# Performance work log

Hardware: AMD Instinct MI355X
Metric: run time of the kernel (lower is better)

## Reference

```python
import jax, jax.numpy as jnp
import numpy as np

D = 1024      # feature_dim / vertice_dim
H = 4         # n_heads
HD = D // H   # head dim 256
DFF = 2 * D   # 2048
DV = 1024     # vertice_dim
T = 64        # frame_num
PERIOD = 30
NEG = -1e9


def setup_inputs() -> dict:
    key = jax.random.key(0)
    ks = iter(jax.random.split(key, 32))
    sc = 0.02
    def w(shape):
        return jax.random.normal(next(ks), shape, dtype=jnp.float32) * sc
    return {
        "hidden_states": jax.random.normal(next(ks), (T, DV), dtype=jnp.float32),
        "hid_w": w((D, DV)), "hid_b": w((D,)),
        "obj_w": w((D, 80)),
        "sa_in_w": w((3 * D, D)), "sa_in_b": w((3 * D,)),
        "sa_out_w": w((D, D)), "sa_out_b": w((D,)),
        "ca_in_w": w((3 * D, D)), "ca_in_b": w((3 * D,)),
        "ca_out_w": w((D, D)), "ca_out_b": w((D,)),
        "ln1_g": jnp.ones((D,), jnp.float32), "ln1_b": jnp.zeros((D,), jnp.float32),
        "ln2_g": jnp.ones((D,), jnp.float32), "ln2_b": jnp.zeros((D,), jnp.float32),
        "ln3_g": jnp.ones((D,), jnp.float32), "ln3_b": jnp.zeros((D,), jnp.float32),
        "ff1_w": w((DFF, D)), "ff1_b": w((DFF,)),
        "ff2_w": w((D, DFF)), "ff2_b": w((D,)),
        "vr_w": w((DV, D)), "vr_b": w((DV,)),
        "vm_w": w((D, DV)), "vm_b": w((D,)),
    }


def _periodic_pe():
    # sin/cos PE over one period, tiled (PeriodicPositionalEncoding)
    pos = jnp.arange(PERIOD, dtype=jnp.float32)[:, None]
    div = jnp.exp(jnp.arange(0, D, 2, dtype=jnp.float32) * (-np.log(10000.0) / D))
    pe = jnp.zeros((PERIOD, D), jnp.float32)
    pe = pe.at[:, 0::2].set(jnp.sin(pos * div)).at[:, 1::2].set(jnp.cos(pos * div))
    reps = T // PERIOD + 1
    return jnp.tile(pe, (reps, 1))[:T]  # (T, D)


def reference(hidden_states, hid_w, hid_b, obj_w,
              sa_in_w, sa_in_b, sa_out_w, sa_out_b,
              ca_in_w, ca_in_b, ca_out_w, ca_out_b,
              ln1_g, ln1_b, ln2_g, ln2_b, ln3_g, ln3_b,
              ff1_w, ff1_b, ff2_w, ff2_b, vr_w, vr_b, vm_w, vm_b):
    mem = hidden_states @ hid_w.T + hid_b          # (S=T, D)
    style = obj_w[:, 0]                             # one-hot(0) @ obj_vector
    pe = _periodic_pe()

    # ALiBi-style biased causal mask (init_biased_mask, n_head=4)
    slopes = 0.25 ** jnp.arange(1, H + 1, dtype=jnp.float32)
    idx = jnp.arange(T)
    i_, j_ = idx[:, None], idx[None, :]
    alibi = -((i_ - j_) // PERIOD).astype(jnp.float32)
    tgt_bias = jnp.where(j_ <= i_, slopes[:, None, None] * alibi[None], NEG)  # (H,T,T)
    # vocaset enc_dec_mask: frame i may only attend memory frame i
    mem_bias = jnp.where(i_ == j_, 0.0, NEG)  # (T,S)

    def mha(q_in, kv_in, in_w, in_b, out_w, out_b, bias):
        wq, wk, wv = jnp.split(in_w, 3, axis=0)
        bq, bk, bv = jnp.split(in_b, 3)
        q = (q_in @ wq.T + bq).reshape(-1, H, HD)
        k = (kv_in @ wk.T + bk).reshape(-1, H, HD)
        v = (kv_in @ wv.T + bv).reshape(-1, H, HD)
        s = jnp.einsum('qhd,khd->hqk', q, k) / np.sqrt(HD) + bias
        a = jax.nn.softmax(s, axis=-1)
        o = jnp.einsum('hqk,khd->qhd', a, v).reshape(-1, D)
        return o @ out_w.T + out_b

    def ln(x, g, b):
        m = x.mean(-1, keepdims=True)
        v = ((x - m) ** 2).mean(-1, keepdims=True)
        return (x - m) / jnp.sqrt(v + 1e-5) * g + b

    def decode(x):  # post-norm TransformerDecoderLayer (eval, dropout off)
        x = ln(x + mha(x, x, sa_in_w, sa_in_b, sa_out_w, sa_out_b, tgt_bias), ln1_g, ln1_b)
        x = ln(x + mha(x, mem, ca_in_w, ca_in_b, ca_out_w, ca_out_b, mem_bias[None]), ln2_g, ln2_b)
        h = jax.nn.relu(x @ ff1_w.T + ff1_b) @ ff2_w.T + ff2_b
        return ln(x + h, ln3_g, ln3_b)

    # independent of the zero-padded future slots, matching the growing-seq loop.
    emb0 = jnp.zeros((T, D), jnp.float32).at[0].set(style)

    def step(emb, i):
        out = decode(emb + pe)
        new_tok = (out[i] @ vr_w.T + vr_b) @ vm_w.T + vm_b + style
        return emb.at[i + 1].set(new_tok), None

    emb, _ = jax.lax.scan(step, emb0, jnp.arange(T - 1))
    # final iteration's vertice_out over the full T-length sequence
    return decode(emb + pe) @ vr_w.T + vr_b  # (T, DV)
```

## Files before the change

### kernel.cpp

```cpp
#include <hip/hip_runtime.h>
#include <math.h>

#define DIM  1024
#define SEQ  64
#define HDIM 256
#define NBLK 256

__device__ __forceinline__ float wsum(float v){
  v += __shfl_xor(v, 32, 64); v += __shfl_xor(v, 16, 64); v += __shfl_xor(v, 8, 64);
  v += __shfl_xor(v, 4, 64);  v += __shfl_xor(v, 2, 64);  v += __shfl_xor(v, 1, 64);
  return v;
}
__device__ __forceinline__ float wmax(float v){
  v = fmaxf(v, __shfl_xor(v, 32, 64)); v = fmaxf(v, __shfl_xor(v, 16, 64));
  v = fmaxf(v, __shfl_xor(v, 8, 64));  v = fmaxf(v, __shfl_xor(v, 4, 64));
  v = fmaxf(v, __shfl_xor(v, 2, 64));  v = fmaxf(v, __shfl_xor(v, 1, 64));
  return v;
}
__device__ __forceinline__ float2 breduce2(float va, float vb, float* red){
  int tid = threadIdx.x;
  va = wsum(va); vb = wsum(vb);
  if ((tid & 63) == 0){ red[(tid >> 6) * 2] = va; red[(tid >> 6) * 2 + 1] = vb; }
  __syncthreads();
  float ra = red[0] + red[2] + red[4] + red[6];
  float rb = red[1] + red[3] + red[5] + red[7];
  __syncthreads();
  return make_float2(ra, rb);
}

__device__ __forceinline__ float ldc(const float* p){
  return __hip_atomic_load(p, __ATOMIC_RELAXED, __HIP_MEMORY_SCOPE_AGENT);
}
__device__ __forceinline__ void stc(float* p, float v){
  __hip_atomic_store(p, v, __ATOMIC_RELAXED, __HIP_MEMORY_SCOPE_AGENT);
}

__device__ __forceinline__ void spin_ge(unsigned* p, unsigned ep){
  unsigned spins = 0;
  while (__hip_atomic_load(p, __ATOMIC_RELAXED, __HIP_MEMORY_SCOPE_AGENT) < ep){
    if (++spins > 4194304u){
      unsigned s2 = 0;
      while (__hip_atomic_load(p, __ATOMIC_ACQUIRE, __HIP_MEMORY_SCOPE_AGENT) < ep){
        __builtin_amdgcn_s_sleep(2);
        if (++s2 > 100000000u) break;
      }
      return;
    }
  }
}

#define SLOT_STRIDE 32
__device__ __forceinline__ void gsync(unsigned* slots, unsigned ep, int bid, int tid){
  asm volatile("s_waitcnt vmcnt(0)" ::: "memory");
  __syncthreads();
  if (tid == 0)
    __hip_atomic_store(&slots[bid * SLOT_STRIDE], ep, __ATOMIC_RELAXED, __HIP_MEMORY_SCOPE_AGENT);
  spin_ge(&slots[tid * SLOT_STRIDE], ep);
  __syncthreads();
  asm volatile("" ::: "memory");
}

__global__ void matmul_nn_1024(const float* __restrict__ A, const float* __restrict__ B,
                               float* __restrict__ Cc){
  __shared__ float As[32][33];
  __shared__ float Bs[32][33];
  int tb = blockIdx.x * 32, ta = blockIdx.y * 32;
  int tx = threadIdx.x & 31, ty = threadIdx.x >> 5;
  float acc[4] = {0.f, 0.f, 0.f, 0.f};
  for (int k0 = 0; k0 < 1024; k0 += 32){
    for (int r = ty; r < 32; r += 8) As[r][tx] = A[(size_t)(ta + r) * 1024 + k0 + tx];
    for (int r = ty; r < 32; r += 8) Bs[r][tx] = B[(size_t)(k0 + r) * 1024 + tb + tx];
    __syncthreads();
    #pragma unroll
    for (int kk = 0; kk < 32; ++kk){
      float bv = Bs[kk][tx];
      #pragma unroll
      for (int m = 0; m < 4; ++m) acc[m] = fmaf(As[ty + 8 * m][kk], bv, acc[m]);
    }
    __syncthreads();
  }
  for (int m = 0; m < 4; ++m) Cc[(size_t)(ta + ty + 8 * m) * 1024 + tb + tx] = acc[m];
}

struct CoopArgs {
  const float *hs, *hid_w, *hid_b;
  const float *sa_in_w, *sa_in_b, *sa_out_w, *sa_out_b;
  const float *ca_in_w, *ca_in_b, *ca_out_w, *ca_out_b;
  const float *ln1_g, *ln1_b, *ln2_g, *ln2_b, *ln3_g, *ln3_b;
  const float *ff1_w, *ff1_b, *ff2_w, *ff2_b;
  const float *vr_w, *vr_b, *vm_w, *vm_b, *obj_w;
  const float *Cm;
  float *pe, *emb, *kc, *vc, *mem, *vtmp, *cac, *q, *u, *hb, *w, *s;
  float *out;
  unsigned *bar;
  unsigned *flags;
};

__global__ void __launch_bounds__(256, 2) decode_loop(CoopArgs a){
  const int tid = threadIdx.x, bid = blockIdx.x;
  const int wave = tid >> 6, lane = tid & 63;
  const int gw = bid * 4 + wave;
  __shared__ float sm[2048];
  __shared__ float scp[256];
  __shared__ float red[8];
  unsigned* slots = a.bar;
  unsigned ep = 0;

  const float NLOG = -9.210340371976184f / 1024.0f;
  const float divw = __expf((float)(2 * (gw >> 1)) * NLOG);
  const int parw = gw & 1;

  {
    float pw[16];
    const float* pr = a.hid_w + (size_t)gw * DIM;
    #pragma unroll
    for (int k = 0; k < 16; ++k) pw[k] = pr[lane + 64 * k];
    float bias = a.hid_b[gw];
    for (int t = 0; t < 64; ++t){
      const float* xr = a.hs + (size_t)t * DIM;
      float acc = 0.f;
      #pragma unroll
      for (int k = 0; k < 16; ++k) acc = fmaf(pw[k], xr[lane + 64 * k], acc);
      acc = wsum(acc);
      if (lane == 0) stc(a.mem + (size_t)t * DIM + gw, acc + bias);
    }
    {
      float arg = (float)(lane % 30) * divw;
      float pev = parw ? cosf(arg) : sinf(arg);
      stc(a.pe + (size_t)lane * DIM + gw, pev);
    }
    if (bid == 0){
      for (int d = tid; d < DIM; d += 256) stc(a.emb + d, a.obj_w[(size_t)d * 80]);
    }
  }
  ++ep; gsync(slots, ep, bid, tid);

  {
    float pw[16];
    const float* pr = a.ca_in_w + (size_t)(2 * DIM + gw) * DIM;
    #pragma unroll
    for (int k = 0; k < 16; ++k) pw[k] = pr[lane + 64 * k];
    float bias = a.ca_in_b[2 * DIM + gw];
    for (int t = 0; t < 64; ++t){
      const float* xr = a.mem + (size_t)t * DIM;
      #pragma unroll
      for (int k = 0; k < 4; ++k) sm[tid + 256 * k] = ldc(xr + tid + 256 * k);
      __syncthreads();
      float acc = 0.f;
      #pragma unroll
      for (int k = 0; k < 16; ++k) acc = fmaf(pw[k], sm[lane + 64 * k], acc);
      acc = wsum(acc);
      if (lane == 0) stc(a.vtmp + (size_t)t * DIM + gw, acc + bias);
      __syncthreads();
    }
  }
  ++ep; gsync(slots, ep, bid, tid);

  {
    float pw[16];
    const float* pr = a.ca_out_w + (size_t)gw * DIM;
    #pragma unroll
    for (int k = 0; k < 16; ++k) pw[k] = pr[lane + 64 * k];
    float bias = a.ca_out_b[gw];
    for (int t = 0; t < 64; ++t){
      const float* xr = a.vtmp + (size_t)t * DIM;
      #pragma unroll
      for (int k = 0; k < 4; ++k) sm[tid + 256 * k] = ldc(xr + tid + 256 * k);
      __syncthreads();
      float acc = 0.f;
      #pragma unroll
      for (int k = 0; k < 16; ++k) acc = fmaf(pw[k], sm[lane + 64 * k], acc);
      acc = wsum(acc);
      if (lane == 0) stc(a.cac + (size_t)t * DIM + gw, acc + bias);
      __syncthreads();
    }
  }
  ++ep; gsync(slots, ep, bid, tid);

  float wq[16], wk[16], wv[16], wo[16], f1a[16], f1b[16], f2[32];
  {
    const float* pq = a.sa_in_w + (size_t)gw * DIM;
    const float* pk = a.sa_in_w + (size_t)(DIM + gw) * DIM;
    const float* pv = a.sa_in_w + (size_t)(2 * DIM + gw) * DIM;
    const float* po = a.sa_out_w + (size_t)gw * DIM;
    const float* p1a = a.ff1_w + (size_t)(2 * gw) * DIM;
    const float* p1b = a.ff1_w + (size_t)(2 * gw + 1) * DIM;
    const float* p2 = a.ff2_w + (size_t)gw * 2048;
    #pragma unroll
    for (int k = 0; k < 16; ++k){
      int d = lane + 64 * k;
      wq[k] = pq[d]; wk[k] = pk[d]; wv[k] = pv[d]; wo[k] = po[d];
      f1a[k] = p1a[d]; f1b[k] = p1b[d];
    }
    #pragma unroll
    for (int k = 0; k < 32; ++k) f2[k] = p2[lane + 64 * k];
  }
  const float b_q  = a.sa_in_b[gw];
  const float b_k  = a.sa_in_b[DIM + gw];
  const float b_v  = a.sa_in_b[2 * DIM + gw];
  const float b_o  = a.sa_out_b[gw];
  const float b_1a = a.ff1_b[2 * gw];
  const float b_1b = a.ff1_b[2 * gw + 1];
  const float b_2  = a.ff2_b[gw];
  const float b_vr = a.vr_b[gw];
  float cbv;
  {
    const float* pv = a.vm_w + (size_t)gw * DIM;
    float acc = 0.f;
    #pragma unroll
    for (int k = 0; k < 16; ++k) acc = fmaf(pv[lane + 64 * k], a.vr_b[lane + 64 * k], acc);
    cbv = wsum(acc) + a.vm_b[gw] + a.obj_w[(size_t)gw * 80];
  }

  float c0 = 0.f, c1 = 0.f, c2 = 0.f, c3 = 0.f;

  const bool is_score = (bid < 16);
  const int sc_h  = bid >> 2;
  const int sc_jg = bid & 3;
  const float sc_slope = 1.0f / (float)(4 << (2 * sc_h));

  for (int i = 0; i < SEQ; ++i){
    const float* per = a.pe + (size_t)i * DIM;

    {
      float* xs = sm;
      const float* er = a.emb + (size_t)i * DIM;
      #pragma unroll
      for (int k = 0; k < 4; ++k){
        int d = tid + 256 * k;
        xs[d] = ldc(er + d) + ldc(per + d);
      }
      __syncthreads();
      float aq = 0.f, ak = 0.f, av = 0.f;
      #pragma unroll
      for (int k = 0; k < 16; ++k){
        float x = xs[lane + 64 * k];
        aq = fmaf(wq[k], x, aq);
        ak = fmaf(wk[k], x, ak);
        av = fmaf(wv[k], x, av);
      }
      aq = wsum(aq); ak = wsum(ak); av = wsum(av);
      if (lane == 0){
        stc(a.q + gw, aq + b_q);
        stc(a.kc + (size_t)i * DIM + gw, ak + b_k);
        stc(a.vc + (size_t)i * DIM + gw, av + b_v);
      }
      __syncthreads();
    }
    ++ep; gsync(slots, ep, bid, tid);

    {
      float* xs  = sm;
      float* qsl = sm + 1024;
      float remb = ldc(a.emb + (size_t)i * DIM + gw);
      #pragma unroll
      for (int k = 0; k < 4; ++k) xs[tid + 256 * k] = ldc(a.vc + (size_t)i * DIM + tid + 256 * k);
      if (is_score) qsl[tid] = ldc(a.q + sc_h * HDIM + tid);
      __syncthreads();
      float p0 = 0.f, p1 = 0.f, p2 = 0.f, p3 = 0.f;
      #pragma unroll
      for (int k = 0; k < 4; ++k){
        p0 = fmaf(wo[k],      xs[lane + 64 * k],        p0);
        p1 = fmaf(wo[k + 4],  xs[lane + 64 * (k + 4)],  p1);
        p2 = fmaf(wo[k + 8],  xs[lane + 64 * (k + 8)],  p2);
        p3 = fmaf(wo[k + 12], xs[lane + 64 * (k + 12)], p3);
      }
      p0 = wsum(p0); p1 = wsum(p1); p2 = wsum(p2); p3 = wsum(p3);
      if (lane == i){ c0 = p0; c1 = p1; c2 = p2; c3 = p3; }
      if (is_score){
        #pragma unroll
        for (int jj = 0; jj < 4; ++jj){
          int j = sc_jg * 16 + wave * 4 + jj;
          if (j <= i){
            const float* kr = a.kc + (size_t)j * DIM + sc_h * HDIM;
            float acc = 0.f;
            #pragma unroll
            for (int m = 0; m < 4; ++m)
              acc = fmaf(qsl[m * 64 + lane], ldc(kr + m * 64 + lane), acc);
            acc = wsum(acc);
            if (lane == 0)
              stc(a.s + sc_h * 64 + j, acc * 0.0625f - sc_slope * (float)((i - j) / 30));
          }
        }
        asm volatile("s_waitcnt vmcnt(0)" ::: "memory");
        __syncthreads();
        if (tid == 0)
          __hip_atomic_store(&a.flags[bid * SLOT_STRIDE], (unsigned)(i + 1),
                             __ATOMIC_RELAXED, __HIP_MEMORY_SCOPE_AGENT);
      }
      if (tid < 16) spin_ge(&a.flags[tid * SLOT_STRIDE], (unsigned)(i + 1));
      __syncthreads();
      {
        const int h = wave;
        float sv = (lane <= i) ? ldc(a.s + h * 64 + lane) : -3.0e38f;
        float mx = wmax(sv);
        float p = (lane <= i) ? __expf(sv - mx) : 0.f;
        float sum = wsum(p);
        scp[h * 64 + lane] = p / sum;
      }
      __syncthreads();
      float t = scp[lane] * c0 + scp[64 + lane] * c1 + scp[128 + lane] * c2 + scp[192 + lane] * c3;
      t = wsum(t);
      if (lane == 0){
        stc(a.u + gw, remb + ldc(per + gw) + t + b_o);
      }
      __syncthreads();
    }
    ++ep; gsync(slots, ep, bid, tid);

    float x2v;
    {
      float* xs = sm;
      #pragma unroll
      for (int k = 0; k < 4; ++k) xs[tid + 256 * k] = ldc(a.u + tid + 256 * k);
      __syncthreads();
      float sa = 0.f, sb = 0.f;
      #pragma unroll
      for (int k = 0; k < 4; ++k){ float x = xs[tid + 256 * k]; sa += x; sb = fmaf(x, x, sb); }
      float2 r = breduce2(sa, sb, red);
      float mean = r.x * (1.f / 1024.f);
      float var = r.y * (1.f / 1024.f) - mean * mean;
      float rs = 1.f / sqrtf(var + 1e-5f);
      float tv[4];
      float ta = 0.f, tb = 0.f;
      #pragma unroll
      for (int k = 0; k < 4; ++k){
        int d = tid + 256 * k;
        float x1 = (xs[d] - mean) * rs * a.ln1_g[d] + a.ln1_b[d];
        tv[k] = x1 + ldc(a.cac + (size_t)i * DIM + d);
        ta += tv[k]; tb = fmaf(tv[k], tv[k], tb);
      }
      float2 r2 = breduce2(ta, tb, red);
      float mean2 = r2.x * (1.f / 1024.f);
      float var2 = r2.y * (1.f / 1024.f) - mean2 * mean2;
      float rs2 = 1.f / sqrtf(var2 + 1e-5f);
      #pragma unroll
      for (int k = 0; k < 4; ++k){
        int d = tid + 256 * k;
        xs[d] = (tv[k] - mean2) * rs2 * a.ln2_g[d] + a.ln2_b[d];
      }
      __syncthreads();
      x2v = xs[gw];
      float acc0 = 0.f, acc1 = 0.f;
      #pragma unroll
      for (int k = 0; k < 16; ++k){
        float x = xs[lane + 64 * k];
        acc0 = fmaf(f1a[k], x, acc0);
        acc1 = fmaf(f1b[k], x, acc1);
      }
      acc0 = wsum(acc0); acc1 = wsum(acc1);
      if (lane == 0){
        stc(a.hb + 2 * gw,     fmaxf(acc0 + b_1a, 0.f));
        stc(a.hb + 2 * gw + 1, fmaxf(acc1 + b_1b, 0.f));
      }
      __syncthreads();
    }
    ++ep; gsync(slots, ep, bid, tid);

    float vrr[16], cmr[16];
    {
      float* hsm = sm;
      #pragma unroll
      for (int k = 0; k < 8; ++k) hsm[tid + 256 * k] = ldc(a.hb + tid + 256 * k);
      const float* pr = a.vr_w + (size_t)gw * DIM;
      const float* pc = a.Cm + (size_t)gw * DIM;
      #pragma unroll
      for (int k = 0; k < 16; ++k){ vrr[k] = pr[lane + 64 * k]; cmr[k] = pc[lane + 64 * k]; }
      __syncthreads();
      float acc = 0.f;
      #pragma unroll
      for (int k = 0; k < 32; ++k) acc = fmaf(f2[k], hsm[lane + 64 * k], acc);
      acc = wsum(acc);
      if (lane == 0) stc(a.w + gw, x2v + acc + b_2);
      __syncthreads();
    }
    ++ep; gsync(slots, ep, bid, tid);

    {
      float* xs = sm;
      #pragma unroll
      for (int k = 0; k < 4; ++k) xs[tid + 256 * k] = ldc(a.w + tid + 256 * k);
      __syncthreads();
      float sa = 0.f, sb = 0.f;
      #pragma unroll
      for (int k = 0; k < 4; ++k){ float x = xs[tid + 256 * k]; sa += x; sb = fmaf(x, x, sb); }
      float2 r = breduce2(sa, sb, red);
      float mean = r.x * (1.f / 1024.f);
      float var = r.y * (1.f / 1024.f) - mean * mean;
      float rs = 1.f / sqrtf(var + 1e-5f);
      float ov[4];
      #pragma unroll
      for (int k = 0; k < 4; ++k){
        int d = tid + 256 * k;
        ov[k] = (xs[d] - mean) * rs * a.ln3_g[d] + a.ln3_b[d];
      }
      __syncthreads();
      #pragma unroll
      for (int k = 0; k < 4; ++k) xs[tid + 256 * k] = ov[k];
      __syncthreads();
      {
        float ar = 0.f, ac = 0.f;
        #pragma unroll
        for (int k = 0; k < 16; ++k){
          float x = xs[lane + 64 * k];
          ar = fmaf(vrr[k], x, ar);
          ac = fmaf(cmr[k], x, ac);
        }
        ar = wsum(ar); ac = wsum(ac);
        if (lane == 0){
          a.out[(size_t)i * DIM + gw] = ar + b_vr;
          if (i < SEQ - 1) stc(a.emb + (size_t)(i + 1) * DIM + gw, ac + cbv);
        }
      }
      __syncthreads();
    }
    ++ep; gsync(slots, ep, bid, tid);
  }
}

extern "C" void kernel_launch(void* const* d_in, const int* in_sizes, int n_in,
                              void* d_out, int out_size, void* d_ws, size_t ws_size,
                              hipStream_t stream){
  const float* hs       = (const float*)d_in[0];
  const float* hid_w    = (const float*)d_in[1];
  const float* hid_b    = (const float*)d_in[2];
  const float* obj_w    = (const float*)d_in[3];
  const float* sa_in_w  = (const float*)d_in[4];
  const float* sa_in_b  = (const float*)d_in[5];
  const float* sa_out_w = (const float*)d_in[6];
  const float* sa_out_b = (const float*)d_in[7];
  const float* ca_in_w  = (const float*)d_in[8];
  const float* ca_in_b  = (const float*)d_in[9];
  const float* ca_out_w = (const float*)d_in[10];
  const float* ca_out_b = (const float*)d_in[11];
  const float* ln1_g    = (const float*)d_in[12];
  const float* ln1_b    = (const float*)d_in[13];
  const float* ln2_g    = (const float*)d_in[14];
  const float* ln2_b    = (const float*)d_in[15];
  const float* ln3_g    = (const float*)d_in[16];
  const float* ln3_b    = (const float*)d_in[17];
  const float* ff1_w    = (const float*)d_in[18];
  const float* ff1_b    = (const float*)d_in[19];
  const float* ff2_w    = (const float*)d_in[20];
  const float* ff2_b    = (const float*)d_in[21];
  const float* vr_w     = (const float*)d_in[22];
  const float* vr_b     = (const float*)d_in[23];
  const float* vm_w     = (const float*)d_in[24];
  const float* vm_b     = (const float*)d_in[25];

  float* ws = (float*)d_ws;
  float* pe   = ws;
  float* emb  = ws + 65536;
  float* kc   = ws + 131072;
  float* vc   = ws + 196608;
  float* mem  = ws + 262144;
  float* vtmp = ws + 327680;
  float* cac  = ws + 393216;
  float* Cm   = ws + 458752;
  float* q    = ws + 1507328;
  float* u    = ws + 1508352;
  float* hb   = ws + 1509376;
  float* wv   = ws + 1511424;
  float* sbuf = ws + 1512448;
  unsigned* bar   = (unsigned*)(ws + 1513472);
  unsigned* flags = bar + 256 * SLOT_STRIDE;

  hipMemsetAsync((void*)bar, 0, (256 + 16) * SLOT_STRIDE * 4, stream);

  matmul_nn_1024<<<dim3(32, 32), 256, 0, stream>>>(vm_w, vr_w, Cm);

  CoopArgs A;
  A.hs = hs; A.hid_w = hid_w; A.hid_b = hid_b;
  A.sa_in_w = sa_in_w; A.sa_in_b = sa_in_b; A.sa_out_w = sa_out_w; A.sa_out_b = sa_out_b;
  A.ca_in_w = ca_in_w; A.ca_in_b = ca_in_b; A.ca_out_w = ca_out_w; A.ca_out_b = ca_out_b;
  A.ln1_g = ln1_g; A.ln1_b = ln1_b; A.ln2_g = ln2_g; A.ln2_b = ln2_b; A.ln3_g = ln3_g; A.ln3_b = ln3_b;
  A.ff1_w = ff1_w; A.ff1_b = ff1_b; A.ff2_w = ff2_w; A.ff2_b = ff2_b;
  A.vr_w = vr_w; A.vr_b = vr_b; A.vm_w = vm_w; A.vm_b = vm_b; A.obj_w = obj_w;
  A.Cm = Cm;
  A.pe = pe; A.emb = emb; A.kc = kc; A.vc = vc; A.mem = mem; A.vtmp = vtmp; A.cac = cac;
  A.q = q; A.u = u; A.hb = hb; A.w = wv; A.s = sbuf;
  A.out = (float*)d_out;
  A.bar = bar; A.flags = flags;

  void* params[1] = { &A };
  hipError_t e = hipLaunchCooperativeKernel((void*)decode_loop, dim3(NBLK), dim3(256), params, 0, stream);
  if (e != hipSuccess){
    decode_loop<<<dim3(NBLK), dim3(256), 0, stream>>>(A);
  }
}
```

Baseline: 2.176 ms.

## Fold QKV projection into token-generation weights to drop a grid sync per step

Precomputes fused weights WqF/WkF/WvF = sa_in_w·(vm_w·vr_w) and projects the periodic PE, style and constant bias through the QKV weights once up front. The next step's q/k/v can then be produced in the same phase that emits the output token, which removes the per-step QKV phase and its grid-wide barrier. It also simplifies the spin-wait fallback and keeps only the current-step V row. The costs are an extra 3x1024^3 folding GEMM before the loop, more register pressure from holding the fused rows, and a changed floating-point association order.

New measurement: 2.461 ms. 1.13x slower.

```diff
diff --git a/kernel.cpp b/kernel.cpp
--- a/kernel.cpp
+++ b/kernel.cpp
@@ -5,6 +5,7 @@
 #define SEQ  64
 #define HDIM 256
 #define NBLK 256
+#define SLOT_STRIDE 32
 
 __device__ __forceinline__ float wsum(float v){
   v += __shfl_xor(v, 32, 64); v += __shfl_xor(v, 16, 64); v += __shfl_xor(v, 8, 64);
@@ -34,22 +35,12 @@
 __device__ __forceinline__ void stc(float* p, float v){
   __hip_atomic_store(p, v, __ATOMIC_RELAXED, __HIP_MEMORY_SCOPE_AGENT);
 }
-
 __device__ __forceinline__ void spin_ge(unsigned* p, unsigned ep){
   unsigned spins = 0;
   while (__hip_atomic_load(p, __ATOMIC_RELAXED, __HIP_MEMORY_SCOPE_AGENT) < ep){
-    if (++spins > 4194304u){
-      unsigned s2 = 0;
-      while (__hip_atomic_load(p, __ATOMIC_ACQUIRE, __HIP_MEMORY_SCOPE_AGENT) < ep){
-        __builtin_amdgcn_s_sleep(2);
-        if (++s2 > 100000000u) break;
-      }
-      return;
-    }
-  }
-}
-
-#define SLOT_STRIDE 32
+    if (++spins > 100000000u) break;
+  }
+}
 __device__ __forceinline__ void gsync(unsigned* slots, unsigned ep, int bid, int tid){
   asm volatile("s_waitcnt vmcnt(0)" ::: "memory");
   __syncthreads();
@@ -81,6 +72,29 @@
   }
   for (int m = 0; m < 4; ++m) Cc[(size_t)(ta + ty + 8 * m) * 1024 + tb + tx] = acc[m];
 }
+__global__ void fold3_1024(const float* __restrict__ A0, const float* __restrict__ B,
+                           float* __restrict__ W0){
+  __shared__ float As[32][33];
+  __shared__ float Bs[32][33];
+  const float* A = A0 + (size_t)blockIdx.z * 1024 * 1024;
+  float* Cc = W0 + (size_t)blockIdx.z * 1024 * 1024;
+  int tb = blockIdx.x * 32, ta = blockIdx.y * 32;
+  int tx = threadIdx.x & 31, ty = threadIdx.x >> 5;
+  float acc[4] = {0.f, 0.f, 0.f, 0.f};
+  for (int k0 = 0; k0 < 1024; k0 += 32){
+    for (int r = ty; r < 32; r += 8) As[r][tx] = A[(size_t)(ta + r) * 1024 + k0 + tx];
+    for (int r = ty; r < 32; r += 8) Bs[r][tx] = B[(size_t)(k0 + r) * 1024 + tb + tx];
+    __syncthreads();
+    #pragma unroll
+    for (int kk = 0; kk < 32; ++kk){
+      float bv = Bs[kk][tx];
+      #pragma unroll
+      for (int m = 0; m < 4; ++m) acc[m] = fmaf(As[ty + 8 * m][kk], bv, acc[m]);
+    }
+    __syncthreads();
+  }
+  for (int m = 0; m < 4; ++m) Cc[(size_t)(ta + ty + 8 * m) * 1024 + tb + tx] = acc[m];
+}
 
 struct CoopArgs {
   const float *hs, *hid_w, *hid_b;
@@ -89,26 +103,24 @@
   const float *ln1_g, *ln1_b, *ln2_g, *ln2_b, *ln3_g, *ln3_b;
   const float *ff1_w, *ff1_b, *ff2_w, *ff2_b;
   const float *vr_w, *vr_b, *vm_w, *vm_b, *obj_w;
-  const float *Cm;
-  float *pe, *emb, *kc, *vc, *mem, *vtmp, *cac, *q, *u, *hb, *w, *s;
+  const float *Cm, *WqF, *WkF, *WvF;
+  float *mem, *vtmp, *cac, *kc, *vcur, *q, *u, *hb, *w, *s;
+  float *peT, *stylev, *cbvec, *wqpeT, *wkpeT, *wvpeT;
   float *out;
-  unsigned *bar;
-  unsigned *flags;
+  unsigned *bar, *flags;
 };
 
 __global__ void __launch_bounds__(256, 2) decode_loop(CoopArgs a){
   const int tid = threadIdx.x, bid = blockIdx.x;
   const int wave = tid >> 6, lane = tid & 63;
   const int gw = bid * 4 + wave;
-  __shared__ float sm[2048];
+  __shared__ float smA[2048];
+  __shared__ float smB[1024];
+  __shared__ float smC[1024];
   __shared__ float scp[256];
   __shared__ float red[8];
-  unsigned* slots = a.bar;
-  unsigned ep = 0;
-
+  unsigned bep = 0;
   const float NLOG = -9.210340371976184f / 1024.0f;
-  const float divw = __expf((float)(2 * (gw >> 1)) * NLOG);
-  const int parw = gw & 1;
 
   {
     float pw[16];
@@ -124,17 +136,29 @@
       acc = wsum(acc);
       if (lane == 0) stc(a.mem + (size_t)t * DIM + gw, acc + bias);
     }
-    {
-      float arg = (float)(lane % 30) * divw;
-      float pev = parw ? cosf(arg) : sinf(arg);
-      stc(a.pe + (size_t)lane * DIM + gw, pev);
-    }
-    if (bid == 0){
-      for (int d = tid; d < DIM; d += 256) stc(a.emb + d, a.obj_w[(size_t)d * 80]);
-    }
-  }
-  ++ep; gsync(slots, ep, bid, tid);
-
+    if (bid < 30){
+      int p = bid;
+      for (int d = tid; d < DIM; d += 256){
+        float dv = __expf((float)(2 * (d >> 1)) * NLOG);
+        float arg = (float)p * dv;
+        stc(a.peT + (size_t)p * DIM + d, (d & 1) ? cosf(arg) : sinf(arg));
+      }
+    } else if (bid == 30){
+      for (int d = tid; d < DIM; d += 256) stc(a.stylev + d, a.obj_w[(size_t)d * 80]);
+    }
+  }
+  ++bep; gsync(a.bar, bep, bid, tid);
+
+  float cbv;
+  {
+    const float* pv = a.vm_w + (size_t)gw * DIM;
+    float acc = 0.f;
+    #pragma unroll
+    for (int k = 0; k < 16; ++k) acc = fmaf(pv[lane + 64 * k], a.vr_b[lane + 64 * k], acc);
+    acc = wsum(acc);
+    cbv = acc + a.vm_b[gw] + ldc(a.stylev + gw);
+    if (lane == 0) stc(a.cbvec + gw, cbv);
+  }
   {
     float pw[16];
     const float* pr = a.ca_in_w + (size_t)(2 * DIM + gw) * DIM;
@@ -144,17 +168,17 @@
     for (int t = 0; t < 64; ++t){
       const float* xr = a.mem + (size_t)t * DIM;
       #pragma unroll
-      for (int k = 0; k < 4; ++k) sm[tid + 256 * k] = ldc(xr + tid + 256 * k);
+      for (int k = 0; k < 4; ++k) smA[tid + 256 * k] = ldc(xr + tid + 256 * k);
       __syncthreads();
       float acc = 0.f;
       #pragma unroll
-      for (int k = 0; k < 16; ++k) acc = fmaf(pw[k], sm[lane + 64 * k], acc);
+      for (int k = 0; k < 16; ++k) acc = fmaf(pw[k], smA[lane + 64 * k], acc);
       acc = wsum(acc);
       if (lane == 0) stc(a.vtmp + (size_t)t * DIM + gw, acc + bias);
       __syncthreads();
     }
   }
-  ++ep; gsync(slots, ep, bid, tid);
+  ++bep; gsync(a.bar, bep, bid, tid);
 
   {
     float pw[16];
@@ -165,23 +189,83 @@
     for (int t = 0; t < 64; ++t){
       const float* xr = a.vtmp + (size_t)t * DIM;
       #pragma unroll
-      for (int k = 0; k < 4; ++k) sm[tid + 256 * k] = ldc(xr + tid + 256 * k);
+      for (int k = 0; k < 4; ++k) smA[tid + 256 * k] = ldc(xr + tid + 256 * k);
       __syncthreads();
       float acc = 0.f;
       #pragma unroll
-      for (int k = 0; k < 16; ++k) acc = fmaf(pw[k], sm[lane + 64 * k], acc);
+      for (int k = 0; k < 16; ++k) acc = fmaf(pw[k], smA[lane + 64 * k], acc);
       acc = wsum(acc);
       if (lane == 0) stc(a.cac + (size_t)t * DIM + gw, acc + bias);
       __syncthreads();
     }
   }
-  ++ep; gsync(slots, ep, bid, tid);
-
-  float wq[16], wk[16], wv[16], wo[16], f1a[16], f1b[16], f2[32];
+  ++bep; gsync(a.bar, bep, bid, tid);
+
+  float aqcb, akcb, avcb, aq0, ak0, av0;
   {
+    float wqr[16], wkr[16], wvr[16];
     const float* pq = a.sa_in_w + (size_t)gw * DIM;
     const float* pk = a.sa_in_w + (size_t)(DIM + gw) * DIM;
     const float* pv = a.sa_in_w + (size_t)(2 * DIM + gw) * DIM;
+    #pragma unroll
+    for (int k = 0; k < 16; ++k){
+      int d = lane + 64 * k;
+      wqr[k] = pq[d]; wkr[k] = pk[d]; wvr[k] = pv[d];
+    }
+    const float b_q = a.sa_in_b[gw];
+    const float b_k = a.sa_in_b[DIM + gw];
+    const float b_v = a.sa_in_b[2 * DIM + gw];
+    #pragma unroll
+    for (int k = 0; k < 4; ++k) smA[tid + 256 * k] = ldc(a.cbvec + tid + 256 * k);
+    __syncthreads();
+    float dq = 0.f, dk = 0.f, dv = 0.f;
+    #pragma unroll
+    for (int k = 0; k < 16; ++k){
+      float x = smA[lane + 64 * k];
+      dq = fmaf(wqr[k], x, dq); dk = fmaf(wkr[k], x, dk); dv = fmaf(wvr[k], x, dv);
+    }
+    aqcb = wsum(dq) + b_q; akcb = wsum(dk) + b_k; avcb = wsum(dv) + b_v;
+    __syncthreads();
+    #pragma unroll
+    for (int k = 0; k < 4; ++k) smA[tid + 256 * k] = ldc(a.stylev + tid + 256 * k);
+    __syncthreads();
+    float sq = 0.f, sk = 0.f, sv = 0.f;
+    #pragma unroll
+    for (int k = 0; k < 16; ++k){
+      float x = smA[lane + 64 * k];
+      sq = fmaf(wqr[k], x, sq); sk = fmaf(wkr[k], x, sk); sv = fmaf(wvr[k], x, sv);
+    }
+    sq = wsum(sq); sk = wsum(sk); sv = wsum(sv);
+    __syncthreads();
+    float pq0 = 0.f, pk0 = 0.f, pv0 = 0.f;
+    for (int p = 0; p < 30; ++p){
+      #pragma unroll
+      for (int k = 0; k < 4; ++k) smA[tid + 256 * k] = ldc(a.peT + (size_t)p * DIM + tid + 256 * k);
+      __syncthreads();
+      float tq = 0.f, tk = 0.f, tv = 0.f;
+      #pragma unroll
+      for (int k = 0; k < 16; ++k){
+        float x = smA[lane + 64 * k];
+        tq = fmaf(wqr[k], x, tq); tk = fmaf(wkr[k], x, tk); tv = fmaf(wvr[k], x, tv);
+      }
+      tq = wsum(tq); tk = wsum(tk); tv = wsum(tv);
+      if (lane == 0){
+        stc(a.wqpeT + (size_t)p * DIM + gw, tq);
+        stc(a.wkpeT + (size_t)p * DIM + gw, tk);
+        stc(a.wvpeT + (size_t)p * DIM + gw, tv);
+      }
+      if (p == 0){ pq0 = tq; pk0 = tk; pv0 = tv; }
+      __syncthreads();
+    }
+    aq0 = sq + pq0 + b_q; ak0 = sk + pk0 + b_k; av0 = sv + pv0 + b_v;
+  }
+  ++bep; gsync(a.bar, bep, bid, tid);
+
+  float fq[16], fk[16], fv[16], wo[16], f1a[16], f1b[16], f2[32];
+  {
+    const float* pq = a.WqF + (size_t)gw * DIM;
+    const float* pk = a.WkF + (size_t)gw * DIM;
+    const float* pv = a.WvF + (size_t)gw * DIM;
     const float* po = a.sa_out_w + (size_t)gw * DIM;
     const float* p1a = a.ff1_w + (size_t)(2 * gw) * DIM;
     const float* p1b = a.ff1_w + (size_t)(2 * gw + 1) * DIM;
@@ -189,81 +273,51 @@
     #pragma unroll
     for (int k = 0; k < 16; ++k){
       int d = lane + 64 * k;
-      wq[k] = pq[d]; wk[k] = pk[d]; wv[k] = pv[d]; wo[k] = po[d];
+      fq[k] = pq[d]; fk[k] = pk[d]; fv[k] = pv[d]; wo[k] = po[d];
       f1a[k] = p1a[d]; f1b[k] = p1b[d];
     }
     #pragma unroll
     for (int k = 0; k < 32; ++k) f2[k] = p2[lane + 64 * k];
   }
-  const float b_q  = a.sa_in_b[gw];
-  const float b_k  = a.sa_in_b[DIM + gw];
-  const float b_v  = a.sa_in_b[2 * DIM + gw];
   const float b_o  = a.sa_out_b[gw];
   const float b_1a = a.ff1_b[2 * gw];
   const float b_1b = a.ff1_b[2 * gw + 1];
   const float b_2  = a.ff2_b[gw];
   const float b_vr = a.vr_b[gw];
-  float cbv;
-  {
-    const float* pv = a.vm_w + (size_t)gw * DIM;
-    float acc = 0.f;
-    #pragma unroll
-    for (int k = 0; k < 16; ++k) acc = fmaf(pv[lane + 64 * k], a.vr_b[lane + 64 * k], acc);
-    cbv = wsum(acc) + a.vm_b[gw] + a.obj_w[(size_t)gw * 80];
-  }
 
   float c0 = 0.f, c1 = 0.f, c2 = 0.f, c3 = 0.f;
-
   const bool is_score = (bid < 16);
   const int sc_h  = bid >> 2;
   const int sc_jg = bid & 3;
   const float sc_slope = 1.0f / (float)(4 << (2 * sc_h));
 
+  float xres;
+  if (lane == 0){
+    stc(a.q + gw, aq0);
+    stc(a.kc + gw, ak0);
+    stc(a.vcur + gw, av0);
+  }
+  xres = a.obj_w[(size_t)gw * 80] + ldc(a.peT + gw);
+  ++bep; gsync(a.bar, bep, bid, tid);
+
+  float vrr[16], cmr[16];
   for (int i = 0; i < SEQ; ++i){
-    const float* per = a.pe + (size_t)i * DIM;
+    const unsigned ep = (unsigned)(i + 1);
 
     {
-      float* xs = sm;
-      const float* er = a.emb + (size_t)i * DIM;
       #pragma unroll
       for (int k = 0; k < 4; ++k){
-        int d = tid + 256 * k;
-        xs[d] = ldc(er + d) + ldc(per + d);
-      }
-      __syncthreads();
-      float aq = 0.f, ak = 0.f, av = 0.f;
-      #pragma unroll
-      for (int k = 0; k < 16; ++k){
-        float x = xs[lane + 64 * k];
-        aq = fmaf(wq[k], x, aq);
-        ak = fmaf(wk[k], x, ak);
-        av = fmaf(wv[k], x, av);
-      }
-      aq = wsum(aq); ak = wsum(ak); av = wsum(av);
-      if (lane == 0){
-        stc(a.q + gw, aq + b_q);
-        stc(a.kc + (size_t)i * DIM + gw, ak + b_k);
-        stc(a.vc + (size_t)i * DIM + gw, av + b_v);
-      }
-      __syncthreads();
-    }
-    ++ep; gsync(slots, ep, bid, tid);
-
-    {
-      float* xs  = sm;
-      float* qsl = sm + 1024;
-      float remb = ldc(a.emb + (size_t)i * DIM + gw);
-      #pragma unroll
-      for (int k = 0; k < 4; ++k) xs[tid + 256 * k] = ldc(a.vc + (size_t)i * DIM + tid + 256 * k);
-      if (is_score) qsl[tid] = ldc(a.q + sc_h * HDIM + tid);
+        smB[tid + 256 * k] = ldc(a.vcur + tid + 256 * k);
+        smC[tid + 256 * k] = ldc(a.q + tid + 256 * k);
+      }
       __syncthreads();
       float p0 = 0.f, p1 = 0.f, p2 = 0.f, p3 = 0.f;
       #pragma unroll
       for (int k = 0; k < 4; ++k){
-        p0 = fmaf(wo[k],      xs[lane + 64 * k],        p0);
-        p1 = fmaf(wo[k + 4],  xs[lane + 64 * (k + 4)],  p1);
-        p2 = fmaf(wo[k + 8],  xs[lane + 64 * (k + 8)],  p2);
-        p3 = fmaf(wo[k + 12], xs[lane + 64 * (k + 12)], p3);
+        p0 = fmaf(wo[k],      smB[lane + 64 * k],        p0);
+        p1 = fmaf(wo[k + 4],  smB[lane + 64 * (k + 4)],  p1);
+        p2 = fmaf(wo[k + 8],  smB[lane + 64 * (k + 8)],  p2);
+        p3 = fmaf(wo[k + 12], smB[lane + 64 * (k + 12)], p3);
       }
       p0 = wsum(p0); p1 = wsum(p1); p2 = wsum(p2); p3 = wsum(p3);
       if (lane == i){ c0 = p0; c1 = p1; c2 = p2; c3 = p3; }
@@ -276,7 +330,7 @@
             float acc = 0.f;
             #pragma unroll
             for (int m = 0; m < 4; ++m)
-              acc = fmaf(qsl[m * 64 + lane], ldc(kr + m * 64 + lane), acc);
+              acc = fmaf(smC[sc_h * HDIM + m * 64 + lane], ldc(kr + m * 64 + lane), acc);
             acc = wsum(acc);
             if (lane == 0)
               stc(a.s + sc_h * 64 + j, acc * 0.0625f - sc_slope * (float)((i - j) / 30));
@@ -285,10 +339,10 @@
         asm volatile("s_waitcnt vmcnt(0)" ::: "memory");
         __syncthreads();
         if (tid == 0)
-          __hip_atomic_store(&a.flags[bid * SLOT_STRIDE], (unsigned)(i + 1),
+          __hip_atomic_store(&a.flags[bid * SLOT_STRIDE], ep,
                              __ATOMIC_RELAXED, __HIP_MEMORY_SCOPE_AGENT);
       }
-      if (tid < 16) spin_ge(&a.flags[tid * SLOT_STRIDE], (unsigned)(i + 1));
+      if (tid < 16) spin_ge(&a.flags[tid * SLOT_STRIDE], ep);
       __syncthreads();
       {
         const int h = wave;
@@ -301,50 +355,50 @@
       __syncthreads();
       float t = scp[lane] * c0 + scp[64 + lane] * c1 + scp[128 + lane] * c2 + scp[192 + lane] * c3;
       t = wsum(t);
-      if (lane == 0){
-        stc(a.u + gw, remb + ldc(per + gw) + t + b_o);
-      }
-      __syncthreads();
-    }
-    ++ep; gsync(slots, ep, bid, tid);
+      if (lane == 0) stc(a.u + gw, xres + t + b_o);
+      __syncthreads();
+    }
+    ++bep; gsync(a.bar, bep, bid, tid);
 
     float x2v;
     {
-      float* xs = sm;
-      #pragma unroll
-      for (int k = 0; k < 4; ++k) xs[tid + 256 * k] = ldc(a.u + tid + 256 * k);
+      float cr[4];
+      #pragma unroll
+      for (int k = 0; k < 4; ++k) cr[k] = ldc(a.cac + (size_t)i * DIM + tid + 256 * k);
+      #pragma unroll
+      for (int k = 0; k < 4; ++k) smA[tid + 256 * k] = ldc(a.u + tid + 256 * k);
       __syncthreads();
       float sa = 0.f, sb = 0.f;
       #pragma unroll
-      for (int k = 0; k < 4; ++k){ float x = xs[tid + 256 * k]; sa += x; sb = fmaf(x, x, sb); }
+      for (int k = 0; k < 4; ++k){ float x = smA[tid + 256 * k]; sa += x; sb = fmaf(x, x, sb); }
       float2 r = breduce2(sa, sb, red);
       float mean = r.x * (1.f / 1024.f);
-      float var = r.y * (1.f / 1024.f) - mean * mean;
+      float var  = r.y * (1.f / 1024.f) - mean * mean;
       float rs = 1.f / sqrtf(var + 1e-5f);
       float tv[4];
       float ta = 0.f, tb = 0.f;
       #pragma unroll
       for (int k = 0; k < 4; ++k){
         int d = tid + 256 * k;
-        float x1 = (xs[d] - mean) * rs * a.ln1_g[d] + a.ln1_b[d];
-        tv[k] = x1 + ldc(a.cac + (size_t)i * DIM + d);
+        float x1 = (smA[d] - mean) * rs * a.ln1_g[d] + a.ln1_b[d];
+        tv[k] = x1 + cr[k];
         ta += tv[k]; tb = fmaf(tv[k], tv[k], tb);
       }
-      float2 r2 = breduce2(ta, tb, red);
-      float mean2 = r2.x * (1.f / 1024.f);
-      float var2 = r2.y * (1.f / 1024.f) - mean2 * mean2;
+      float2 r2v = breduce2(ta, tb, red);
+      float mean2 = r2v.x * (1.f / 1024.f);
+      float var2  = r2v.y * (1.f / 1024.f) - mean2 * mean2;
       float rs2 = 1.f / sqrtf(var2 + 1e-5f);
       #pragma unroll
       for (int k = 0; k < 4; ++k){
         int d = tid + 256 * k;
-        xs[d] = (tv[k] - mean2) * rs2 * a.ln2_g[d] + a.ln2_b[d];
-      }
-      __syncthreads();
-      x2v = xs[gw];
+        smA[d] = (tv[k] - mean2) * rs2 * a.ln2_g[d] + a.ln2_b[d];
+      }
+      __syncthreads();
+      x2v = smA[gw];
       float acc0 = 0.f, acc1 = 0.f;
       #pragma unroll
       for (int k = 0; k < 16; ++k){
-        float x = xs[lane + 64 * k];
+        float x = smA[lane + 64 * k];
         acc0 = fmaf(f1a[k], x, acc0);
         acc1 = fmaf(f1b[k], x, acc1);
       }
@@ -355,66 +409,74 @@
       }
       __syncthreads();
     }
-    ++ep; gsync(slots, ep, bid, tid);
-
-    float vrr[16], cmr[16];
+    ++bep; gsync(a.bar, bep, bid, tid);
+
     {
-      float* hsm = sm;
-      #pragma unroll
-      for (int k = 0; k < 8; ++k) hsm[tid + 256 * k] = ldc(a.hb + tid + 256 * k);
       const float* pr = a.vr_w + (size_t)gw * DIM;
       const float* pc = a.Cm + (size_t)gw * DIM;
       #pragma unroll
       for (int k = 0; k < 16; ++k){ vrr[k] = pr[lane + 64 * k]; cmr[k] = pc[lane + 64 * k]; }
+      #pragma unroll
+      for (int k = 0; k < 8; ++k) smA[tid + 256 * k] = ldc(a.hb + tid + 256 * k);
       __syncthreads();
       float acc = 0.f;
       #pragma unroll
-      for (int k = 0; k < 32; ++k) acc = fmaf(f2[k], hsm[lane + 64 * k], acc);
+      for (int k = 0; k < 32; ++k) acc = fmaf(f2[k], smA[lane + 64 * k], acc);
       acc = wsum(acc);
       if (lane == 0) stc(a.w + gw, x2v + acc + b_2);
       __syncthreads();
     }
-    ++ep; gsync(slots, ep, bid, tid);
+    ++bep; gsync(a.bar, bep, bid, tid);
 
     {
-      float* xs = sm;
-      #pragma unroll
-      for (int k = 0; k < 4; ++k) xs[tid + 256 * k] = ldc(a.w + tid + 256 * k);
+      #pragma unroll
+      for (int k = 0; k < 4; ++k) smA[tid + 256 * k] = ldc(a.w + tid + 256 * k);
       __syncthreads();
       float sa = 0.f, sb = 0.f;
       #pragma unroll
-      for (int k = 0; k < 4; ++k){ float x = xs[tid + 256 * k]; sa += x; sb = fmaf(x, x, sb); }
+      for (int k = 0; k < 4; ++k){ float x = smA[tid + 256 * k]; sa += x; sb = fmaf(x, x, sb); }
       float2 r = breduce2(sa, sb, red);
       float mean = r.x * (1.f / 1024.f);
-      float var = r.y * (1.f / 1024.f) - mean * mean;
+      float var  = r.y * (1.f / 1024.f) - mean * mean;
       float rs = 1.f / sqrtf(var + 1e-5f);
       float ov[4];
       #pragma unroll
       for (int k = 0; k < 4; ++k){
         int d = tid + 256 * k;
-        ov[k] = (xs[d] - mean) * rs * a.ln3_g[d] + a.ln3_b[d];
-      }
-      __syncthreads();
-      #pragma unroll
-      for (int k = 0; k < 4; ++k) xs[tid + 256 * k] = ov[k];
-      __syncthreads();
-      {
-        float ar = 0.f, ac = 0.f;
-        #pragma unroll
-        for (int k = 0; k < 16; ++k){
-          float x = xs[lane + 64 * k];
-          ar = fmaf(vrr[k], x, ar);
-          ac = fmaf(cmr[k], x, ac);
+        ov[k] = (smA[d] - mean) * rs * a.ln3_g[d] + a.ln3_b[d];
+      }
+      __syncthreads();
+      #pragma unroll
+      for (int k = 0; k < 4; ++k) smA[tid + 256 * k] = ov[k];
+      __syncthreads();
+      float ar = 0.f, ac = 0.f, aqn = 0.f, akn = 0.f, avn = 0.f;
+      #pragma unroll
+      for (int k = 0; k < 16; ++k){
+        float x = smA[lane + 64 * k];
+        ar  = fmaf(vrr[k], x, ar);
+        ac  = fmaf(cmr[k], x, ac);
+        aqn = fmaf(fq[k], x, aqn);
+        akn = fmaf(fk[k], x, akn);
+        avn = fmaf(fv[k], x, avn);
+      }
+      ar = wsum(ar); ac = wsum(ac);
+      aqn = wsum(aqn); akn = wsum(akn); avn = wsum(avn);
+      if (lane == 0) a.out[(size_t)i * DIM + gw] = ar + b_vr;
+      if (i < SEQ - 1){
+        int pn = (i + 1) % 30;
+        if (lane == 0){
+          float tq = ldc(a.wqpeT + (size_t)pn * DIM + gw);
+          float tk = ldc(a.wkpeT + (size_t)pn * DIM + gw);
+          float tv = ldc(a.wvpeT + (size_t)pn * DIM + gw);
+          stc(a.q + gw, aqn + aqcb + tq);
+          stc(a.kc + (size_t)(i + 1) * DIM + gw, akn + akcb + tk);
+          stc(a.vcur + gw, avn + avcb + tv);
         }
-        ar = wsum(ar); ac = wsum(ac);
-        if (lane == 0){
-          a.out[(size_t)i * DIM + gw] = ar + b_vr;
-          if (i < SEQ - 1) stc(a.emb + (size_t)(i + 1) * DIM + gw, ac + cbv);
-        }
-      }
-      __syncthreads();
-    }
-    ++ep; gsync(slots, ep, bid, tid);
+        xres = ac + cbv + ldc(a.peT + (size_t)pn * DIM + gw);
+        __syncthreads();
+        ++bep; gsync(a.bar, bep, bid, tid);
+      }
+    }
   }
 }
 
@@ -449,25 +511,33 @@
   const float* vm_b     = (const float*)d_in[25];
 
   float* ws = (float*)d_ws;
-  float* pe   = ws;
-  float* emb  = ws + 65536;
-  float* kc   = ws + 131072;
-  float* vc   = ws + 196608;
-  float* mem  = ws + 262144;
-  float* vtmp = ws + 327680;
-  float* cac  = ws + 393216;
-  float* Cm   = ws + 458752;
-  float* q    = ws + 1507328;
-  float* u    = ws + 1508352;
-  float* hb   = ws + 1509376;
-  float* wv   = ws + 1511424;
-  float* sbuf = ws + 1512448;
-  unsigned* bar   = (unsigned*)(ws + 1513472);
+  float* mem    = ws;
+  float* vtmp   = ws + 65536;
+  float* cac    = ws + 131072;
+  float* kc     = ws + 196608;
+  float* vcur   = ws + 262144;
+  float* q      = ws + 263168;
+  float* u      = ws + 264192;
+  float* hb     = ws + 265216;
+  float* wv     = ws + 267264;
+  float* sbuf   = ws + 268288;
+  float* peT    = ws + 269312;
+  float* stylev = ws + 300032;
+  float* cbvec  = ws + 301056;
+  float* wqpeT  = ws + 302080;
+  float* wkpeT  = ws + 332800;
+  float* wvpeT  = ws + 363520;
+  unsigned* bar   = (unsigned*)(ws + 394240);
   unsigned* flags = bar + 256 * SLOT_STRIDE;
+  float* Cm     = ws + 409600;
+  float* WqF    = ws + 1458176;
+  float* WkF    = ws + 2506752;
+  float* WvF    = ws + 3555328;
 
   hipMemsetAsync((void*)bar, 0, (256 + 16) * SLOT_STRIDE * 4, stream);
 
   matmul_nn_1024<<<dim3(32, 32), 256, 0, stream>>>(vm_w, vr_w, Cm);
+  fold3_1024<<<dim3(32, 32, 3), 256, 0, stream>>>(sa_in_w, Cm, WqF);
 
   CoopArgs A;
   A.hs = hs; A.hid_w = hid_w; A.hid_b = hid_b;
@@ -476,9 +546,11 @@
   A.ln1_g = ln1_g; A.ln1_b = ln1_b; A.ln2_g = ln2_g; A.ln2_b = ln2_b; A.ln3_g = ln3_g; A.ln3_b = ln3_b;
   A.ff1_w = ff1_w; A.ff1_b = ff1_b; A.ff2_w = ff2_w; A.ff2_b = ff2_b;
   A.vr_w = vr_w; A.vr_b = vr_b; A.vm_w = vm_w; A.vm_b = vm_b; A.obj_w = obj_w;
-  A.Cm = Cm;
-  A.pe = pe; A.emb = emb; A.kc = kc; A.vc = vc; A.mem = mem; A.vtmp = vtmp; A.cac = cac;
+  A.Cm = Cm; A.WqF = WqF; A.WkF = WkF; A.WvF = WvF;
+  A.mem = mem; A.vtmp = vtmp; A.cac = cac; A.kc = kc; A.vcur = vcur;
   A.q = q; A.u = u; A.hb = hb; A.w = wv; A.s = sbuf;
+  A.peT = peT; A.stylev = stylev; A.cbvec = cbvec;
+  A.wqpeT = wqpeT; A.wkpeT = wkpeT; A.wvpeT = wvpeT;
   A.out = (float*)d_out;
   A.bar = bar; A.flags = flags;
 
```
